# Kernel tuning notes

Hardware: AMD Instinct MI355X
Metric: run time of the kernel (lower is better)

The kernel has to match this reference:

```python
import jax, jax.numpy as jnp
import numpy as np

NUM_HEADS = 16
EMBED_DIM = 1024
HEAD_DIM = EMBED_DIM // NUM_HEADS  # 64
TGT_LEN = 2048
BSZ = 2
SCALE_FACTOR = 1.0
LOCAL_WINDOW = 128


def _make_sinusoidal_pos():
    # (bsz, tgt_len, head_dim): sin in first half of last dim, cos in second half
    pos = np.arange(TGT_LEN, dtype=np.float32)[:, None]
    inv_freq = 1.0 / (10000.0 ** (np.arange(0, HEAD_DIM, 2, dtype=np.float32) / HEAD_DIM))
    ang = pos * inv_freq[None, :]  # (T, D/2)
    sp = np.concatenate([np.sin(ang), np.cos(ang)], axis=-1)  # (T, D)
    return jnp.asarray(np.broadcast_to(sp[None], (BSZ, TGT_LEN, HEAD_DIM)).copy())


def _make_local_mask():
    # True = masked out; band of width +/-LOCAL_WINDOW is visible
    i = np.arange(TGT_LEN)
    band = np.abs(i[:, None] - i[None, :]) > LOCAL_WINDOW  # (T, T)
    mask = np.broadcast_to(band[None], (BSZ * NUM_HEADS, TGT_LEN, TGT_LEN)).copy()
    return jnp.asarray(mask)


def setup_inputs() -> dict:
    key = jax.random.key(0)
    k1, k2, k3, k4, k5 = jax.random.split(key, 5)
    w_scale = 0.02
    return {
        "query": jax.random.normal(k1, (TGT_LEN, BSZ, EMBED_DIM), dtype=jnp.float32),
        "sinusoidal_pos": _make_sinusoidal_pos(),
        "in_proj_weight": jax.random.normal(k2, (3 * EMBED_DIM, EMBED_DIM), dtype=jnp.float32) * w_scale,
        "in_proj_bias": jax.random.normal(k3, (3 * EMBED_DIM,), dtype=jnp.float32) * w_scale,
        "out_proj_weight": jax.random.normal(k4, (EMBED_DIM, EMBED_DIM), dtype=jnp.float32) * w_scale,
        "out_proj_bias": jax.random.normal(k5, (EMBED_DIM,), dtype=jnp.float32) * w_scale,
        "local_attn_mask": _make_local_mask(),
    }


def _apply_rotary(x, sin_pos, cos_pos):
    # rotate_half: (-x1, x0, -x3, x2, ...)
    rot = jnp.stack([-x[..., 1::2], x[..., ::2]], axis=-1).reshape(x.shape)
    return x * cos_pos + rot * sin_pos


def reference(query, sinusoidal_pos, in_proj_weight, in_proj_bias,
              out_proj_weight, out_proj_bias, local_attn_mask):
    T, B, E = query.shape
    H, D = NUM_HEADS, HEAD_DIM
    scaling = float(D * SCALE_FACTOR) ** -0.5

    qkv = query @ in_proj_weight.T + in_proj_bias  # (T, B, 3E)
    q, k, v = jnp.split(qkv, 3, axis=-1)
    q = q * scaling

    # (T, B, E) -> (B*H, T, D), flat index = b*H + h (torch view ordering)
    def to_heads(x):
        return x.reshape(T, B * H, D).transpose(1, 0, 2)

    q, k, v = to_heads(q), to_heads(k), to_heads(v)

    # torch: sinusoidal_pos.repeat(num_heads, 1, 1) -> (H*B, T, D), tile ordering
    sp = jnp.tile(sinusoidal_pos, (H, 1, 1))
    sin, cos = jnp.split(sp, 2, axis=-1)            # each (B*H, T, D/2)
    sin_pos = jnp.repeat(sin, 2, axis=-1)           # s0,s0,s1,s1,...
    cos_pos = jnp.repeat(cos, 2, axis=-1)

    rq = _apply_rotary(q, sin_pos, cos_pos)
    rk = _apply_rotary(k, sin_pos, cos_pos)

    # local (rotary) attention branch with band mask
    local_scores = jnp.einsum('btd,bsd->bts', rq, rk)
    local_scores = jnp.where(local_attn_mask, -jnp.inf, local_scores)
    local_weights = jax.nn.softmax(local_scores, axis=-1)
    local_out = jnp.einsum('bts,bsd->btd', local_weights, v)

    # global attention branch (unmasked)
    scores = jnp.einsum('btd,bsd->bts', q, k)
    weights = jax.nn.softmax(scores, axis=-1)
    attn_out = jnp.einsum('bts,bsd->btd', weights, v) + local_out

    # (B*H, T, D) -> (T, B, E)
    attn_out = attn_out.transpose(1, 0, 2).reshape(T, B, E)
    return attn_out @ out_proj_weight.T + out_proj_bias
```

## Files before the change

### kernel.cpp

```cpp
#include <hip/hip_runtime.h>
#include <cstdint>
#include <cstddef>

#define T_LEN 2048
#define NBATCH 2
#define NHEADS 16
#define HDIM 64
#define EDIM 1024
#define WIN 128
#define QB 128
#define KB 64

typedef float f32;
typedef unsigned short u16;
typedef __attribute__((ext_vector_type(8))) short bf16x8;
typedef __attribute__((ext_vector_type(4))) float f32x4;

__device__ __forceinline__ u16 f2bf(float f) {
  union { float f; unsigned u; } v; v.f = f;
  unsigned r = v.u + 0x7FFF + ((v.u >> 16) & 1);
  return (u16)(r >> 16);
}
__device__ __forceinline__ f32 bf2f(u16 h) {
  union { unsigned u; float f; } v; v.u = ((unsigned)h) << 16;
  return v.f;
}

__global__ __launch_bounds__(256)
void f32_to_bf16_kernel(const f32* __restrict__ in, u16* __restrict__ out, int n8) {
  const int i = blockIdx.x * 256 + threadIdx.x;
  if (i >= n8) return;
  const float4 a = ((const float4*)in)[2 * i];
  const float4 b = ((const float4*)in)[2 * i + 1];
  uint4 o;
  o.x = (unsigned)f2bf(a.x) | ((unsigned)f2bf(a.y) << 16);
  o.y = (unsigned)f2bf(a.z) | ((unsigned)f2bf(a.w) << 16);
  o.z = (unsigned)f2bf(b.x) | ((unsigned)f2bf(b.y) << 16);
  o.w = (unsigned)f2bf(b.z) | ((unsigned)f2bf(b.w) << 16);
  ((uint4*)out)[i] = o;
}

__global__ __launch_bounds__(256)
void rotary_kernel(const u16* __restrict__ qbf, const u16* __restrict__ kbf,
                   const f32* __restrict__ sp,
                   u16* __restrict__ rq, u16* __restrict__ rk) {
  const int i = blockIdx.x * 256 + threadIdx.x;
  const int e0 = i * 8;
  const int t = (e0 >> 6) & (T_LEN - 1);
  const int d0 = e0 & 63;
  const int p0 = d0 >> 1;
  f32 s[4], c[4];
#pragma unroll
  for (int j = 0; j < 4; ++j) {
    s[j] = sp[t * 64 + p0 + j];
    c[j] = sp[t * 64 + 32 + p0 + j];
  }
  uint4 qa = *(const uint4*)&qbf[e0];
  uint4 ka = *(const uint4*)&kbf[e0];
  const u16* qp = (const u16*)&qa;
  const u16* kp = (const u16*)&ka;
  u16 ro[8], ko[8];
#pragma unroll
  for (int p = 0; p < 4; ++p) {
    const f32 x0 = bf2f(qp[2 * p]), x1 = bf2f(qp[2 * p + 1]);
    ro[2 * p]     = f2bf(x0 * c[p] - x1 * s[p]);
    ro[2 * p + 1] = f2bf(x1 * c[p] + x0 * s[p]);
    const f32 y0 = bf2f(kp[2 * p]), y1 = bf2f(kp[2 * p + 1]);
    ko[2 * p]     = f2bf(y0 * c[p] - y1 * s[p]);
    ko[2 * p + 1] = f2bf(y1 * c[p] + y0 * s[p]);
  }
  *(uint4*)&rq[e0] = *(const uint4*)ro;
  *(uint4*)&rk[e0] = *(const uint4*)ko;
}

__global__ __launch_bounds__(256)
void qkv_gemm_bf16(const u16* __restrict__ A, const u16* __restrict__ W,
                   const f32* __restrict__ bias,
                   u16* __restrict__ qb, u16* __restrict__ kb, u16* __restrict__ vb) {
  __shared__ u16 As[128][40];
  __shared__ u16 Bs[128][40];
  const int bm = blockIdx.y * 128;
  const int bn = blockIdx.x * 128;
  const int tid = threadIdx.x;
  const int lane = tid & 63;
  const int wave = tid >> 6;
  const int wr = wave >> 1, wc = wave & 1;
  const int fr = lane & 15;
  const int koff = (lane >> 4) << 3;

  int rowS[2], kcS[2];
#pragma unroll
  for (int u = 0; u < 2; ++u) {
    const int e = tid + u * 256;
    rowS[u] = e >> 2;
    kcS[u] = (e & 3) << 3;
  }

  f32x4 acc[4][4];
#pragma unroll
  for (int m = 0; m < 4; ++m)
#pragma unroll
    for (int n = 0; n < 4; ++n) acc[m][n] = (f32x4){0.f, 0.f, 0.f, 0.f};

  uint4 ra[2], rb[2];
#pragma unroll
  for (int u = 0; u < 2; ++u) {
    ra[u] = *(const uint4*)&A[(size_t)(bm + rowS[u]) * 1024 + kcS[u]];
    rb[u] = *(const uint4*)&W[(size_t)(bn + rowS[u]) * 1024 + kcS[u]];
  }

  for (int kt = 0; kt < 32; ++kt) {
    __syncthreads();
#pragma unroll
    for (int u = 0; u < 2; ++u) {
      *(uint4*)&As[rowS[u]][kcS[u]] = ra[u];
      *(uint4*)&Bs[rowS[u]][kcS[u]] = rb[u];
    }
    __syncthreads();
    if (kt < 31) {
      const int kg = (kt + 1) * 32;
#pragma unroll
      for (int u = 0; u < 2; ++u) {
        ra[u] = *(const uint4*)&A[(size_t)(bm + rowS[u]) * 1024 + kg + kcS[u]];
        rb[u] = *(const uint4*)&W[(size_t)(bn + rowS[u]) * 1024 + kg + kcS[u]];
      }
    }
    bf16x8 af[4], bf[4];
#pragma unroll
    for (int m = 0; m < 4; ++m) af[m] = *(const bf16x8*)&As[wr * 64 + m * 16 + fr][koff];
#pragma unroll
    for (int n = 0; n < 4; ++n) bf[n] = *(const bf16x8*)&Bs[wc * 64 + n * 16 + fr][koff];
#pragma unroll
    for (int m = 0; m < 4; ++m)
#pragma unroll
      for (int n = 0; n < 4; ++n)
        acc[m][n] = __builtin_amdgcn_mfma_f32_16x16x32_bf16(af[m], bf[n], acc[m][n], 0, 0, 0);
  }

  const int r4 = (lane >> 4) << 2;
#pragma unroll
  for (int n = 0; n < 4; ++n) {
    const int col = bn + wc * 64 + n * 16 + fr;
    const int sec = col >> 10;
    const int e = col & 1023;
    const int h = e >> 6, d = e & 63;
    const f32 bv = bias[col];
    u16* dst = sec == 0 ? qb : (sec == 1 ? kb : vb);
    const f32 sc = sec == 0 ? 0.125f : 1.0f;
#pragma unroll
    for (int m = 0; m < 4; ++m) {
#pragma unroll
      for (int j = 0; j < 4; ++j) {
        const int grow = bm + wr * 64 + m * 16 + r4 + j;
        const int t = grow >> 1, b = grow & 1;
        dst[(((size_t)((b << 4) + h)) * T_LEN + t) * HDIM + d] = f2bf((acc[m][n][j] + bv) * sc);
      }
    }
  }
}

__global__ __launch_bounds__(512)
void attn_mfma(const u16* __restrict__ qbf, const u16* __restrict__ rqbf,
               const u16* __restrict__ kbf, const u16* __restrict__ rkbf,
               const u16* __restrict__ vbf, u16* __restrict__ obf) {
  __shared__ u16 Ks[64][72];
  __shared__ u16 Krs[64][72];
  __shared__ u16 Vt[64][72];
  __shared__ u16 Ps[128][72];

  const int id = blockIdx.x;
  const int xcd = id & 7;
  const int ord = id >> 3;
  const int bh = xcd * 4 + (ord >> 4);
  const int qt = ord & 15;

  const int tid = threadIdx.x;
  const int lane = tid & 63;
  const int wave = tid >> 6;
  const int fr = lane & 15;
  const int hi = lane >> 4;
  const size_t hb = (size_t)bh * T_LEN * HDIM;
  const int q0 = qt * QB;
  const int strip = wave * 16;

  bf16x8 qf[2], rqf[2];
  {
    const size_t base = hb + (size_t)(q0 + strip + fr) * HDIM + hi * 8;
    qf[0]  = *(const bf16x8*)&qbf[base];
    qf[1]  = *(const bf16x8*)&qbf[base + 32];
    rqf[0] = *(const bf16x8*)&rqbf[base];
    rqf[1] = *(const bf16x8*)&rqbf[base + 32];
  }

  f32x4 og[4], ol[4];
  f32 mg[4], lg[4], ml[4], ll[4];
#pragma unroll
  for (int n = 0; n < 4; ++n) { og[n] = (f32x4){0,0,0,0}; ol[n] = (f32x4){0,0,0,0}; }
#pragma unroll
  for (int j = 0; j < 4; ++j) { mg[j] = 0.f; lg[j] = 0.f; ml[j] = 0.f; ll[j] = 0.f; }

  const int skey = tid >> 3, sdp = (tid & 7) << 3;
  const int vkey = tid & 63, vdg = tid >> 6;

  for (int kt = 0; kt < 32; ++kt) {
    const int kb = kt * KB;
    const bool loc = (kb + KB > q0 - WIN) && (kb <= q0 + QB - 1 + WIN);

    __syncthreads();

    *(uint4*)&Ks[skey][sdp] = *(const uint4*)&kbf[hb + (size_t)(kb + skey) * HDIM + sdp];
    if (loc)
      *(uint4*)&Krs[skey][sdp] = *(const uint4*)&rkbf[hb + (size_t)(kb + skey) * HDIM + sdp];
    {
      uint4 vv = *(const uint4*)&vbf[hb + (size_t)(kb + vkey) * HDIM + vdg * 8];
      const u16* pv = (const u16*)&vv;
#pragma unroll
      for (int i = 0; i < 8; ++i) Vt[vdg * 8 + i][vkey] = pv[i];
    }
    __syncthreads();

    {
      f32x4 sg[4];
#pragma unroll
      for (int n = 0; n < 4; ++n) sg[n] = (f32x4){0,0,0,0};
#pragma unroll
      for (int ks = 0; ks < 2; ++ks)
#pragma unroll
        for (int n = 0; n < 4; ++n) {
          bf16x8 bfr = *(const bf16x8*)&Ks[n * 16 + fr][ks * 32 + hi * 8];
          sg[n] = __builtin_amdgcn_mfma_f32_16x16x32_bf16(qf[ks], bfr, sg[n], 0, 0, 0);
        }
#pragma unroll
      for (int j = 0; j < 4; ++j) {
        f32 rm = fmaxf(fmaxf(sg[0][j], sg[1][j]), fmaxf(sg[2][j], sg[3][j]));
        rm = fmaxf(rm, __shfl_xor(rm, 1));
        rm = fmaxf(rm, __shfl_xor(rm, 2));
        rm = fmaxf(rm, __shfl_xor(rm, 4));
        rm = fmaxf(rm, __shfl_xor(rm, 8));
        const f32 mn = fmaxf(mg[j], rm);
        const f32 fac = __expf(mg[j] - mn);
        f32 rs = 0.f;
#pragma unroll
        for (int n = 0; n < 4; ++n) {
          const f32 p = __expf(sg[n][j] - mn);
          rs += p;
          Ps[strip + hi * 4 + j][n * 16 + fr] = f2bf(p);
        }
        rs += __shfl_xor(rs, 1); rs += __shfl_xor(rs, 2);
        rs += __shfl_xor(rs, 4); rs += __shfl_xor(rs, 8);
        lg[j] = lg[j] * fac + rs;
        mg[j] = mn;
#pragma unroll
        for (int n = 0; n < 4; ++n) og[n][j] *= fac;
      }
#pragma unroll
      for (int ks = 0; ks < 2; ++ks) {
        bf16x8 pa = *(const bf16x8*)&Ps[strip + fr][ks * 32 + hi * 8];
#pragma unroll
        for (int n = 0; n < 4; ++n) {
          bf16x8 vb = *(const bf16x8*)&Vt[n * 16 + fr][ks * 32 + hi * 8];
          og[n] = __builtin_amdgcn_mfma_f32_16x16x32_bf16(pa, vb, og[n], 0, 0, 0);
        }
      }
    }

    if (loc) {
      f32x4 sl[4];
#pragma unroll
      for (int n = 0; n < 4; ++n) sl[n] = (f32x4){0,0,0,0};
#pragma unroll
      for (int ks = 0; ks < 2; ++ks)
#pragma unroll
        for (int n = 0; n < 4; ++n) {
          bf16x8 bfr = *(const bf16x8*)&Krs[n * 16 + fr][ks * 32 + hi * 8];
          sl[n] = __builtin_amdgcn_mfma_f32_16x16x32_bf16(rqf[ks], bfr, sl[n], 0, 0, 0);
        }
#pragma unroll
      for (int n = 0; n < 4; ++n) {
        const int kj = kb + n * 16 + fr;
#pragma unroll
        for (int j = 0; j < 4; ++j) {
          const int dd = (q0 + strip + hi * 4 + j) - kj;
          if (dd > WIN || dd < -WIN) sl[n][j] = -1e30f;
        }
      }
#pragma unroll
      for (int j = 0; j < 4; ++j) {
        f32 rm = fmaxf(fmaxf(sl[0][j], sl[1][j]), fmaxf(sl[2][j], sl[3][j]));
        rm = fmaxf(rm, __shfl_xor(rm, 1));
        rm = fmaxf(rm, __shfl_xor(rm, 2));
        rm = fmaxf(rm, __shfl_xor(rm, 4));
        rm = fmaxf(rm, __shfl_xor(rm, 8));
        const f32 mn = fmaxf(ml[j], rm);
        const f32 fac = __expf(ml[j] - mn);
        f32 rs = 0.f;
#pragma unroll
        for (int n = 0; n < 4; ++n) {
          const f32 p = __expf(sl[n][j] - mn);
          rs += p;
          Ps[strip + hi * 4 + j][n * 16 + fr] = f2bf(p);
        }
        rs += __shfl_xor(rs, 1); rs += __shfl_xor(rs, 2);
        rs += __shfl_xor(rs, 4); rs += __shfl_xor(rs, 8);
        ll[j] = ll[j] * fac + rs;
        ml[j] = mn;
#pragma unroll
        for (int n = 0; n < 4; ++n) ol[n][j] *= fac;
      }
#pragma unroll
      for (int ks = 0; ks < 2; ++ks) {
        bf16x8 pa = *(const bf16x8*)&Ps[strip + fr][ks * 32 + hi * 8];
#pragma unroll
        for (int n = 0; n < 4; ++n) {
          bf16x8 vb = *(const bf16x8*)&Vt[n * 16 + fr][ks * 32 + hi * 8];
          ol[n] = __builtin_amdgcn_mfma_f32_16x16x32_bf16(pa, vb, ol[n], 0, 0, 0);
        }
      }
    }
  }

#pragma unroll
  for (int j = 0; j < 4; ++j) {
    const int row = q0 + strip + hi * 4 + j;
    const f32 ig = 1.0f / lg[j];
    const f32 il = 1.0f / ll[j];
#pragma unroll
    for (int n = 0; n < 4; ++n)
      obf[hb + (size_t)row * HDIM + n * 16 + fr] = f2bf(og[n][j] * ig + ol[n][j] * il);
  }
}

__global__ __launch_bounds__(256)
void out_gemm_bf16(const u16* __restrict__ Abf, const u16* __restrict__ W,
                   const f32* __restrict__ bias, f32* __restrict__ out) {
  __shared__ u16 As[128][40];
  __shared__ u16 Bs[128][40];
  const int bm = blockIdx.y * 128;
  const int bn = blockIdx.x * 128;
  const int tid = threadIdx.x;
  const int lane = tid & 63;
  const int wave = tid >> 6;
  const int wr = wave >> 1, wc = wave & 1;
  const int fr = lane & 15;
  const int koff = (lane >> 4) << 3;

  int rowS[2], kcS[2];
  size_t abase[2];
#pragma unroll
  for (int u = 0; u < 2; ++u) {
    const int e = tid + u * 256;
    rowS[u] = e >> 2;
    kcS[u] = (e & 3) << 3;
    const int m = bm + rowS[u];
    const int t = m >> 1, b = m & 1;
    abase[u] = (((size_t)(b << 4)) * T_LEN + t) * HDIM;
  }

  f32x4 acc[4][4];
#pragma unroll
  for (int m = 0; m < 4; ++m)
#pragma unroll
    for (int n = 0; n < 4; ++n) acc[m][n] = (f32x4){0.f, 0.f, 0.f, 0.f};

  uint4 ra[2], rb[2];
#pragma unroll
  for (int u = 0; u < 2; ++u) {
    const int k = kcS[u];
    ra[u] = *(const uint4*)&Abf[abase[u] + (size_t)(k >> 6) * 131072 + (k & 63)];
    rb[u] = *(const uint4*)&W[(size_t)(bn + rowS[u]) * 1024 + k];
  }

  for (int kt = 0; kt < 32; ++kt) {
    __syncthreads();
#pragma unroll
    for (int u = 0; u < 2; ++u) {
      *(uint4*)&As[rowS[u]][kcS[u]] = ra[u];
      *(uint4*)&Bs[rowS[u]][kcS[u]] = rb[u];
    }
    __syncthreads();
    if (kt < 31) {
      const int kg = (kt + 1) * 32;
#pragma unroll
      for (int u = 0; u < 2; ++u) {
        const int k = kg + kcS[u];
        ra[u] = *(const uint4*)&Abf[abase[u] + (size_t)(k >> 6) * 131072 + (k & 63)];
        rb[u] = *(const uint4*)&W[(size_t)(bn + rowS[u]) * 1024 + k];
      }
    }
    bf16x8 af[4], bf[4];
#pragma unroll
    for (int m = 0; m < 4; ++m) af[m] = *(const bf16x8*)&As[wr * 64 + m * 16 + fr][koff];
#pragma unroll
    for (int n = 0; n < 4; ++n) bf[n] = *(const bf16x8*)&Bs[wc * 64 + n * 16 + fr][koff];
#pragma unroll
    for (int m = 0; m < 4; ++m)
#pragma unroll
      for (int n = 0; n < 4; ++n)
        acc[m][n] = __builtin_amdgcn_mfma_f32_16x16x32_bf16(af[m], bf[n], acc[m][n], 0, 0, 0);
  }

  const int r4 = (lane >> 4) << 2;
#pragma unroll
  for (int n = 0; n < 4; ++n) {
    const int col = bn + wc * 64 + n * 16 + fr;
    const f32 bv = bias[col];
#pragma unroll
    for (int m = 0; m < 4; ++m) {
#pragma unroll
      for (int j = 0; j < 4; ++j) {
        const int grow = bm + wr * 64 + m * 16 + r4 + j;
        out[(size_t)grow * 1024 + col] = acc[m][n][j] + bv;
      }
    }
  }
}

extern "C" void kernel_launch(void* const* d_in, const int* in_sizes, int n_in,
                              void* d_out, int out_size, void* d_ws, size_t ws_size,
                              hipStream_t stream) {
  const f32* query = (const f32*)d_in[0];
  const f32* sp    = (const f32*)d_in[1];
  const f32* win   = (const f32*)d_in[2];
  const f32* bin   = (const f32*)d_in[3];
  const f32* wout  = (const f32*)d_in[4];
  const f32* bout  = (const f32*)d_in[5];
  f32* out = (f32*)d_out;
  char* wsb = (char*)d_ws;

  u16* xbf  = (u16*)(wsb);
  u16* wibf = (u16*)(wsb + (8u << 20));
  u16* wobf = (u16*)(wsb + (14u << 20));
  u16* qbf  = (u16*)(wsb + (16u << 20));
  u16* kbf  = (u16*)(wsb + (24u << 20));
  u16* vbf  = (u16*)(wsb + (32u << 20));
  u16* rqbf = (u16*)(wsb + (40u << 20));
  u16* rkbf = (u16*)(wsb + (48u << 20));
  u16* awbf = xbf;

  f32_to_bf16_kernel<<<2048, 256, 0, stream>>>(query, xbf, 524288);
  f32_to_bf16_kernel<<<1536, 256, 0, stream>>>(win, wibf, 393216);
  f32_to_bf16_kernel<<<512, 256, 0, stream>>>(wout, wobf, 131072);

  qkv_gemm_bf16<<<dim3(24, 32), 256, 0, stream>>>(xbf, wibf, bin, qbf, kbf, vbf);
  rotary_kernel<<<2048, 256, 0, stream>>>(qbf, kbf, sp, rqbf, rkbf);
  attn_mfma<<<512, 512, 0, stream>>>(qbf, rqbf, kbf, rkbf, vbf, awbf);
  out_gemm_bf16<<<dim3(8, 32), 256, 0, stream>>>(awbf, wobf, bout, out);
}
```

Before: 898.7 us.

## Use direct global-to-LDS loads in GEMMs and merge conversion kernels

Both projection GEMMs now stage tiles with global_load_lds (16-byte direct-to-LDS loads) instead of loading into registers and then writing to shared memory. This removes the register prefetch double-buffer and the padded LDS rows. The three f32-to-bf16 conversion launches are merged into one kernel, which saves launch overhead. The trade-offs are unpadded LDS rows that may cause bank conflicts, and the loss of overlap between the next tile's global load and the current tile's MFMAs, since each iteration now waits on its own load.

```diff
diff --git a/kernel.cpp b/kernel.cpp
--- a/kernel.cpp
+++ b/kernel.cpp
@@ -26,18 +26,29 @@
   return v.f;
 }
 
+__device__ __forceinline__ void gload_lds16(const void* g, void* l) {
+  __builtin_amdgcn_global_load_lds(
+      (const __attribute__((address_space(1))) unsigned int*)g,
+      (__attribute__((address_space(3))) unsigned int*)l, 16, 0, 0);
+}
+
 __global__ __launch_bounds__(256)
-void f32_to_bf16_kernel(const f32* __restrict__ in, u16* __restrict__ out, int n8) {
+void cvt_all_kernel(const f32* __restrict__ q, const f32* __restrict__ wi,
+                    const f32* __restrict__ wo,
+                    u16* __restrict__ qo, u16* __restrict__ wio, u16* __restrict__ woo) {
   const int i = blockIdx.x * 256 + threadIdx.x;
-  if (i >= n8) return;
-  const float4 a = ((const float4*)in)[2 * i];
-  const float4 b = ((const float4*)in)[2 * i + 1];
+  const f32* in; u16* out; int j;
+  if (i < 524288)       { in = q;  out = qo;  j = i; }
+  else if (i < 917504)  { in = wi; out = wio; j = i - 524288; }
+  else                  { in = wo; out = woo; j = i - 917504; }
+  const float4 a = ((const float4*)in)[2 * j];
+  const float4 b = ((const float4*)in)[2 * j + 1];
   uint4 o;
   o.x = (unsigned)f2bf(a.x) | ((unsigned)f2bf(a.y) << 16);
   o.y = (unsigned)f2bf(a.z) | ((unsigned)f2bf(a.w) << 16);
   o.z = (unsigned)f2bf(b.x) | ((unsigned)f2bf(b.y) << 16);
   o.w = (unsigned)f2bf(b.z) | ((unsigned)f2bf(b.w) << 16);
-  ((uint4*)out)[i] = o;
+  ((uint4*)out)[j] = o;
 }
 
 __global__ __launch_bounds__(256)
@@ -77,8 +88,8 @@
 void qkv_gemm_bf16(const u16* __restrict__ A, const u16* __restrict__ W,
                    const f32* __restrict__ bias,
                    u16* __restrict__ qb, u16* __restrict__ kb, u16* __restrict__ vb) {
-  __shared__ u16 As[128][40];
-  __shared__ u16 Bs[128][40];
+  __shared__ u16 As[128][32];
+  __shared__ u16 Bs[128][32];
   const int bm = blockIdx.y * 128;
   const int bn = blockIdx.x * 128;
   const int tid = threadIdx.x;
@@ -88,13 +99,8 @@
   const int fr = lane & 15;
   const int koff = (lane >> 4) << 3;
 
-  int rowS[2], kcS[2];
-#pragma unroll
-  for (int u = 0; u < 2; ++u) {
-    const int e = tid + u * 256;
-    rowS[u] = e >> 2;
-    kcS[u] = (e & 3) << 3;
-  }
+  const int srow = lane >> 2;
+  const int skc = (lane & 3) << 3;
 
   f32x4 acc[4][4];
 #pragma unroll
@@ -102,29 +108,18 @@
 #pragma unroll
     for (int n = 0; n < 4; ++n) acc[m][n] = (f32x4){0.f, 0.f, 0.f, 0.f};
 
-  uint4 ra[2], rb[2];
-#pragma unroll
-  for (int u = 0; u < 2; ++u) {
-    ra[u] = *(const uint4*)&A[(size_t)(bm + rowS[u]) * 1024 + kcS[u]];
-    rb[u] = *(const uint4*)&W[(size_t)(bn + rowS[u]) * 1024 + kcS[u]];
-  }
-
   for (int kt = 0; kt < 32; ++kt) {
     __syncthreads();
 #pragma unroll
-    for (int u = 0; u < 2; ++u) {
-      *(uint4*)&As[rowS[u]][kcS[u]] = ra[u];
-      *(uint4*)&Bs[rowS[u]][kcS[u]] = rb[u];
-    }
-    __syncthreads();
-    if (kt < 31) {
-      const int kg = (kt + 1) * 32;
-#pragma unroll
-      for (int u = 0; u < 2; ++u) {
-        ra[u] = *(const uint4*)&A[(size_t)(bm + rowS[u]) * 1024 + kg + kcS[u]];
-        rb[u] = *(const uint4*)&W[(size_t)(bn + rowS[u]) * 1024 + kg + kcS[u]];
-      }
-    }
+    for (int ii = 0; ii < 2; ++ii) {
+      const int q = 2 * wave + ii;
+      const int r = q * 16 + srow;
+      const int kc = kt * 32 + skc;
+      gload_lds16(&A[(size_t)(bm + r) * 1024 + kc], &As[q * 16][0]);
+      gload_lds16(&W[(size_t)(bn + r) * 1024 + kc], &Bs[q * 16][0]);
+    }
+    __syncthreads();
+
     bf16x8 af[4], bf[4];
 #pragma unroll
     for (int m = 0; m < 4; ++m) af[m] = *(const bf16x8*)&As[wr * 64 + m * 16 + fr][koff];
@@ -333,8 +328,8 @@
 __global__ __launch_bounds__(256)
 void out_gemm_bf16(const u16* __restrict__ Abf, const u16* __restrict__ W,
                    const f32* __restrict__ bias, f32* __restrict__ out) {
-  __shared__ u16 As[128][40];
-  __shared__ u16 Bs[128][40];
+  __shared__ u16 As[128][32];
+  __shared__ u16 Bs[128][32];
   const int bm = blockIdx.y * 128;
   const int bn = blockIdx.x * 128;
   const int tid = threadIdx.x;
@@ -344,17 +339,8 @@
   const int fr = lane & 15;
   const int koff = (lane >> 4) << 3;
 
-  int rowS[2], kcS[2];
-  size_t abase[2];
-#pragma unroll
-  for (int u = 0; u < 2; ++u) {
-    const int e = tid + u * 256;
-    rowS[u] = e >> 2;
-    kcS[u] = (e & 3) << 3;
-    const int m = bm + rowS[u];
-    const int t = m >> 1, b = m & 1;
-    abase[u] = (((size_t)(b << 4)) * T_LEN + t) * HDIM;
-  }
+  const int srow = lane >> 2;
+  const int skc = (lane & 3) << 3;
 
   f32x4 acc[4][4];
 #pragma unroll
@@ -362,31 +348,21 @@
 #pragma unroll
     for (int n = 0; n < 4; ++n) acc[m][n] = (f32x4){0.f, 0.f, 0.f, 0.f};
 
-  uint4 ra[2], rb[2];
-#pragma unroll
-  for (int u = 0; u < 2; ++u) {
-    const int k = kcS[u];
-    ra[u] = *(const uint4*)&Abf[abase[u] + (size_t)(k >> 6) * 131072 + (k & 63)];
-    rb[u] = *(const uint4*)&W[(size_t)(bn + rowS[u]) * 1024 + k];
-  }
-
   for (int kt = 0; kt < 32; ++kt) {
-    __syncthreads();
-#pragma unroll
-    for (int u = 0; u < 2; ++u) {
-      *(uint4*)&As[rowS[u]][kcS[u]] = ra[u];
-      *(uint4*)&Bs[rowS[u]][kcS[u]] = rb[u];
-    }
-    __syncthreads();
-    if (kt < 31) {
-      const int kg = (kt + 1) * 32;
-#pragma unroll
-      for (int u = 0; u < 2; ++u) {
-        const int k = kg + kcS[u];
-        ra[u] = *(const uint4*)&Abf[abase[u] + (size_t)(k >> 6) * 131072 + (k & 63)];
-        rb[u] = *(const uint4*)&W[(size_t)(bn + rowS[u]) * 1024 + k];
-      }
-    }
+    const int h = kt >> 1;
+    const int dd = (kt & 1) * 32 + skc;
+    __syncthreads();
+#pragma unroll
+    for (int ii = 0; ii < 2; ++ii) {
+      const int q = 2 * wave + ii;
+      const int r = q * 16 + srow;
+      const int m = bm + r;
+      const int t = m >> 1, b = m & 1;
+      gload_lds16(&Abf[(((size_t)((b << 4) + h)) * T_LEN + t) * HDIM + dd], &As[q * 16][0]);
+      gload_lds16(&W[(size_t)(bn + r) * 1024 + kt * 32 + skc], &Bs[q * 16][0]);
+    }
+    __syncthreads();
+
     bf16x8 af[4], bf[4];
 #pragma unroll
     for (int m = 0; m < 4; ++m) af[m] = *(const bf16x8*)&As[wr * 64 + m * 16 + fr][koff];
@@ -437,10 +413,7 @@
   u16* rkbf = (u16*)(wsb + (48u << 20));
   u16* awbf = xbf;
 
-  f32_to_bf16_kernel<<<2048, 256, 0, stream>>>(query, xbf, 524288);
-  f32_to_bf16_kernel<<<1536, 256, 0, stream>>>(win, wibf, 393216);
-  f32_to_bf16_kernel<<<512, 256, 0, stream>>>(wout, wobf, 131072);
-
+  cvt_all_kernel<<<4096, 256, 0, stream>>>(query, win, wout, xbf, wibf, wobf);
   qkv_gemm_bf16<<<dim3(24, 32), 256, 0, stream>>>(xbf, wibf, bin, qbf, kbf, vbf);
   rotary_kernel<<<2048, 256, 0, stream>>>(qbf, kbf, sp, rqbf, rkbf);
   attn_mfma<<<512, 512, 0, stream>>>(qbf, rqbf, kbf, rkbf, vbf, awbf);
```

Measured after the change: 804.5 us. -10.5%, faster.
